# Kernel optimization log

Measured on AMD Instinct MI355X. Metric: run time of the kernel, lower is better.

The kernel has to match this reference:

```python
import jax, jax.numpy as jnp
import numpy as np

N_NODES = 262144      # 2048 graphs * 128 nodes each
NUM_GRAPHS = 2048
MAX_NODES = 128
HIDDEN = 256
OUT_CH = 12
N_EDGES = 2097152     # ~avg degree 8


def setup_inputs() -> dict:
    key = jax.random.key(0)
    k1, k2, k3, k4 = jax.random.split(key, 4)
    x = jax.random.normal(k1, (N_NODES, HIDDEN), dtype=jnp.float32)
    # xavier-ish projection weight for Linear(6*hidden -> 12)
    W = jax.random.normal(k2, (OUT_CH, 6 * HIDDEN), dtype=jnp.float32) * (1.0 / np.sqrt(6 * HIDDEN))
    b = jnp.zeros((OUT_CH,), dtype=jnp.float32)
    # uniform graphs: sorted batch ids, MAX_NODES nodes per graph
    batch = (jnp.arange(N_NODES, dtype=jnp.int32) // MAX_NODES).astype(jnp.int32)
    # edges sampled within graphs: pick graph, then two local node ids
    g = jax.random.randint(k3, (N_EDGES,), 0, NUM_GRAPHS, dtype=jnp.int32)
    loc = jax.random.randint(k4, (N_EDGES, 2), 0, MAX_NODES, dtype=jnp.int32)
    src = g * MAX_NODES + loc[:, 0]
    dst = g * MAX_NODES + loc[:, 1]
    edge_index = jnp.stack([src, dst], axis=0).astype(jnp.int32)
    return {"x": x, "W": W, "b": b, "batch": batch, "edge_index": edge_index,
            "num_graphs": NUM_GRAPHS, "max_nodes": MAX_NODES}


def reference(x, W, b, batch, edge_index, num_graphs, max_nodes):
    N, H = x.shape
    G, M = num_graphs, max_nodes
    # local index of each node within its graph (batch is sorted by graph)
    counts = jax.ops.segment_sum(jnp.ones((N,), dtype=jnp.int32), batch, num_segments=G)
    starts = jnp.cumsum(counts) - counts            # exclusive prefix sum => first node of each graph
    local = jnp.arange(N, dtype=jnp.int32) - starts[batch]
    # dense per-graph node features X [G, M, H]
    X = jnp.zeros((G, M, H), dtype=x.dtype).at[batch, local].set(x)
    # dense symmetric adjacency A [G, M, M] (assignment semantics, like the torch loop)
    gi = batch[edge_index[0]]
    li = local[edge_index[0]]
    lj = local[edge_index[1]]
    A = jnp.zeros((G, M, M), dtype=x.dtype)
    A = A.at[gi, li, lj].set(1.0)
    A = A.at[gi, lj, li].set(1.0)
    # 6-gram walk readouts
    walk = X
    vs = [walk.sum(axis=1)]                          # v1
    for _ in range(5):                               # v2..v6
        walk = jnp.einsum('gnm,gmh->gnh', A, walk) * X
        vs.append(walk.sum(axis=1))
    out = jnp.concatenate(vs, axis=-1)               # == stack(dim=1).reshape(G, 6*H)
    out = out @ W.T + b                              # n_gram_projection
    return out
```

## Files before the change

### kernel.cpp

```cpp
#include <hip/hip_runtime.h>
#include <stdint.h>

#define NGRAPH 2048
#define MNODES 128
#define HID 256
#define OUTC 12
#define NEDGE 2097152
#define NSUB 16
#define SUBCAP 160
#define CURPAD 16

typedef __attribute__((ext_vector_type(8))) short short8;
typedef __attribute__((ext_vector_type(4))) float v4f;

#define SLICE 64
#define SWT_STRIDE 136

__device__ __forceinline__ unsigned int cvtpk_bf16(float lo, float hi) {
    unsigned int r;
    asm("v_cvt_pk_bf16_f32 %0, %1, %2" : "=v"(r) : "v"(lo), "v"(hi));
    return r;
}

__global__ void scatter_edges(const int* __restrict__ ei,
                              unsigned int* __restrict__ buckets,
                              unsigned int* __restrict__ cursors) {
    int e = blockIdx.x * blockDim.x + threadIdx.x;
    if (e >= NEDGE) return;
    int sub = blockIdx.x & (NSUB - 1);
    int sN = ei[e];
    int dN = ei[NEDGE + e];
    int g = sN >> 7;
    unsigned int slot = atomicAdd(&cursors[(g * NSUB + sub) * CURPAD], 1u);
    if (slot < SUBCAP)
        buckets[((size_t)g * NSUB + sub) * SUBCAP + slot] =
            (unsigned)(sN & 127) | ((unsigned)(dN & 127) << 8);
}

__global__ void build_from_buckets(const unsigned int* __restrict__ buckets,
                                   const unsigned int* __restrict__ cursors,
                                   unsigned int* __restrict__ bits) {
    __shared__ unsigned int sb[MNODES * 4];
    int g = blockIdx.x;
    int t = threadIdx.x;
    for (int i = t; i < MNODES * 4; i += 256) sb[i] = 0;
    __syncthreads();
    int sub = t >> 4;
    int i0 = t & 15;
    unsigned int n = cursors[(g * NSUB + sub) * CURPAD];
    if (n > SUBCAP) n = SUBCAP;
    const unsigned int* bk = buckets + ((size_t)g * NSUB + sub) * SUBCAP;
    for (unsigned int i = i0; i < n; i += 16) {
        unsigned int p = bk[i];
        int li = p & 127;
        int lj = (p >> 8) & 127;
        atomicOr(&sb[li * 4 + (lj >> 5)], 1u << (lj & 31));
        atomicOr(&sb[lj * 4 + (li >> 5)], 1u << (li & 31));
    }
    __syncthreads();
    unsigned int* dst = bits + (size_t)g * (MNODES * 4);
    for (int i = t; i < MNODES * 4; i += 256) dst[i] = sb[i];
}

__global__ void build_bits(const int* __restrict__ ei, unsigned int* __restrict__ bits) {
    int e = blockIdx.x * blockDim.x + threadIdx.x;
    if (e >= NEDGE) return;
    int sN = ei[e];
    int dN = ei[NEDGE + e];
    int g = sN >> 7;
    int li = sN & 127;
    int lj = dN & 127;
    unsigned int* base = bits + (size_t)g * (MNODES * 4);
    atomicOr(&base[li * 4 + (lj >> 5)], 1u << (lj & 31));
    atomicOr(&base[lj * 4 + (li >> 5)], 1u << (li & 31));
}

__launch_bounds__(256, 3)
__global__ void walk2(const float* __restrict__ x,
                      const float* __restrict__ W,
                      const unsigned int* __restrict__ Abits,
                      float* __restrict__ partial) {
    __shared__ unsigned short sWT[2][SLICE][SWT_STRIDE];
    __shared__ float sVs2[2][6][SLICE];

    const int bx = blockIdx.x;
    const int g = bx >> 2;
    const int s = bx & 3;
    const int tid = threadIdx.x;
    const int wave = tid >> 6;
    const int lane = tid & 63;
    const int lrow = lane & 15;
    const int quad = lane >> 4;
    const int rhalf = wave >> 1;
    const int r0 = rhalf * 64;
    const int c0 = (wave & 1) * 32;
    const int cg0 = s * SLICE + c0;

    short8 areg[4][4];
    {
        const uint4* Bg = (const uint4*)(Abits + (size_t)g * (MNODES * 4));
#pragma unroll
        for (int rt = 0; rt < 4; rt++) {
            uint4 w4 = Bg[r0 + rt * 16 + lrow];
#pragma unroll
            for (int ks = 0; ks < 4; ks++) {
                unsigned int w = (ks == 0 ? w4.x : ks == 1 ? w4.y : ks == 2 ? w4.z : w4.w) >> (quad * 8);
                short8 a;
#pragma unroll
                for (int j = 0; j < 8; j++)
                    a[j] = (short)(((w >> j) & 1u) ? 0x3F80 : 0);
                areg[rt][ks] = a;
            }
        }
    }

    float xf[4][2][4];
    const float* xg = x + (size_t)g * (MNODES * HID);
#pragma unroll
    for (int rt = 0; rt < 4; rt++)
#pragma unroll
        for (int ct = 0; ct < 2; ct++) {
            int col = cg0 + ct * 16 + lrow;
#pragma unroll
            for (int reg = 0; reg < 4; reg++) {
                int row = r0 + rt * 16 + quad * 4 + reg;
                xf[rt][ct][reg] = xg[row * HID + col];
            }
        }
#pragma unroll
    for (int ct = 0; ct < 2; ct++) {
        int lcol = c0 + ct * 16 + lrow;
        float cs = 0.0f;
#pragma unroll
        for (int rt = 0; rt < 4; rt++) {
            int nbase = r0 + rt * 16 + quad * 4;
            uint2 u;
            u.x = cvtpk_bf16(xf[rt][ct][0], xf[rt][ct][1]);
            u.y = cvtpk_bf16(xf[rt][ct][2], xf[rt][ct][3]);
            *(uint2*)&sWT[0][lcol][nbase] = u;
            cs += xf[rt][ct][0] + xf[rt][ct][1] + xf[rt][ct][2] + xf[rt][ct][3];
        }
        cs += __shfl_xor(cs, 16);
        cs += __shfl_xor(cs, 32);
        if (quad == 0) sVs2[rhalf][0][lcol] = cs;
    }
    __syncthreads();

    for (int it = 1; it <= 5; it++) {
        const int cur = (it - 1) & 1;
        const int nxt = it & 1;
        v4f acc[4][2];
#pragma unroll
        for (int rt = 0; rt < 4; rt++)
#pragma unroll
            for (int ct = 0; ct < 2; ct++) acc[rt][ct] = (v4f)(0.0f);
#pragma unroll
        for (int ks = 0; ks < 4; ks++) {
            int k0 = ks * 32 + quad * 8;
#pragma unroll
            for (int ct = 0; ct < 2; ct++) {
                short8 bf = *(const short8*)&sWT[cur][c0 + ct * 16 + lrow][k0];
#pragma unroll
                for (int rt = 0; rt < 4; rt++)
                    acc[rt][ct] = __builtin_amdgcn_mfma_f32_16x16x32_bf16(areg[rt][ks], bf, acc[rt][ct], 0, 0, 0);
            }
        }
#pragma unroll
        for (int ct = 0; ct < 2; ct++) {
            int lcol = c0 + ct * 16 + lrow;
            float cs = 0.0f;
#pragma unroll
            for (int rt = 0; rt < 4; rt++) {
                float nw0 = acc[rt][ct][0] * xf[rt][ct][0];
                float nw1 = acc[rt][ct][1] * xf[rt][ct][1];
                float nw2 = acc[rt][ct][2] * xf[rt][ct][2];
                float nw3 = acc[rt][ct][3] * xf[rt][ct][3];
                int nbase = r0 + rt * 16 + quad * 4;
                uint2 u;
                u.x = cvtpk_bf16(nw0, nw1);
                u.y = cvtpk_bf16(nw2, nw3);
                *(uint2*)&sWT[nxt][lcol][nbase] = u;
                cs += nw0 + nw1 + nw2 + nw3;
            }
            cs += __shfl_xor(cs, 16);
            cs += __shfl_xor(cs, 32);
            if (quad == 0) sVs2[rhalf][it][lcol] = cs;
        }
        __syncthreads();
    }

    {
        int cbase = wave * 3;
#pragma unroll
        for (int cc = 0; cc < 3; cc++) {
            int c = cbase + cc;
            const float* wr = W + c * (6 * HID) + s * SLICE;
            float p = 0.0f;
#pragma unroll
            for (int k = 0; k < 6; k++) {
                float v = sVs2[0][k][lane] + sVs2[1][k][lane];
                p += v * wr[k * HID + lane];
            }
#pragma unroll
            for (int off = 32; off >= 1; off >>= 1) p += __shfl_down(p, off);
            if (lane == 0) partial[bx * OUTC + c] = p;
        }
    }
}

__global__ void combine(const float* __restrict__ partial, const float* __restrict__ bvec,
                        float* __restrict__ out) {
    int i = blockIdx.x * blockDim.x + threadIdx.x;
    if (i >= NGRAPH * OUTC) return;
    int c = i % OUTC;
    int g = i / OUTC;
    float p = bvec[c];
#pragma unroll
    for (int s = 0; s < 4; s++) p += partial[(g * 4 + s) * OUTC + c];
    out[i] = p;
}

extern "C" void kernel_launch(void* const* d_in, const int* in_sizes, int n_in,
                              void* d_out, int out_size, void* d_ws, size_t ws_size,
                              hipStream_t stream) {
    const float* x = (const float*)d_in[0];
    const float* W = (const float*)d_in[1];
    const float* b = (const float*)d_in[2];
    const int* ei = (const int*)d_in[4];
    float* out = (float*)d_out;

    const size_t BUCKETS = (size_t)NGRAPH * NSUB * SUBCAP * sizeof(unsigned int);
    const size_t BITS    = (size_t)NGRAPH * MNODES * 4 * sizeof(unsigned int);
    const size_t CURS    = (size_t)NGRAPH * NSUB * CURPAD * sizeof(unsigned int);
    const size_t PARTIAL = (size_t)NGRAPH * 4 * OUTC * sizeof(float);

    if (ws_size >= BUCKETS + BITS + CURS + PARTIAL) {
        unsigned int* buckets = (unsigned int*)d_ws;
        unsigned int* bits    = (unsigned int*)((char*)d_ws + BUCKETS);
        unsigned int* cursors = (unsigned int*)((char*)d_ws + BUCKETS + BITS);
        float* partial        = (float*)((char*)d_ws + BUCKETS + BITS + CURS);
        hipMemsetAsync(cursors, 0, CURS, stream);
        scatter_edges<<<NEDGE / 256, 256, 0, stream>>>(ei, buckets, cursors);
        build_from_buckets<<<NGRAPH, 256, 0, stream>>>(buckets, cursors, bits);
        walk2<<<NGRAPH * 4, 256, 0, stream>>>(x, W, bits, partial);
        combine<<<(NGRAPH * OUTC + 255) / 256, 256, 0, stream>>>(partial, b, out);
    } else {
        unsigned int* bits = (unsigned int*)d_ws;
        float* partial = (float*)((char*)d_ws + BITS);
        hipMemsetAsync(bits, 0, BITS, stream);
        build_bits<<<NEDGE / 512, 512, 0, stream>>>(ei, bits);
        walk2<<<NGRAPH * 4, 256, 0, stream>>>(x, W, bits, partial);
        combine<<<(NGRAPH * OUTC + 255) / 256, 256, 0, stream>>>(partial, b, out);
    }
}
```

Measured before the change: 490.3 us.

## Fuse adjacency bitmap build into walk kernel and use packed f32 math

Removes the separate build_from_buckets kernel. Each walk2 block now builds its graph's adjacency bitmap in shared memory from the edge buckets, reusing one sWT buffer. This drops one launch and the global bits round-trip, at the cost of each graph's buckets being read and OR-ed four times, once per column-slice block. It also switches the elementwise multiply and column sums to v_pk_mul/v_pk_add_f32 and raises wave priority around the MFMA loop with s_setprio.

```diff
diff --git a/kernel.cpp b/kernel.cpp
--- a/kernel.cpp
+++ b/kernel.cpp
@@ -12,6 +12,7 @@
 
 typedef __attribute__((ext_vector_type(8))) short short8;
 typedef __attribute__((ext_vector_type(4))) float v4f;
+typedef __attribute__((ext_vector_type(2))) float v2f;
 
 #define SLICE 64
 #define SWT_STRIDE 136
@@ -20,6 +21,12 @@
     unsigned int r;
     asm("v_cvt_pk_bf16_f32 %0, %1, %2" : "=v"(r) : "v"(lo), "v"(hi));
     return r;
+}
+__device__ __forceinline__ v2f pk_mul(v2f a, v2f b) {
+    v2f r; asm("v_pk_mul_f32 %0, %1, %2" : "=v"(r) : "v"(a), "v"(b)); return r;
+}
+__device__ __forceinline__ v2f pk_add(v2f a, v2f b) {
+    v2f r; asm("v_pk_add_f32 %0, %1, %2" : "=v"(r) : "v"(a), "v"(b)); return r;
 }
 
 __global__ void scatter_edges(const int* __restrict__ ei,
@@ -37,31 +44,6 @@
             (unsigned)(sN & 127) | ((unsigned)(dN & 127) << 8);
 }
 
-__global__ void build_from_buckets(const unsigned int* __restrict__ buckets,
-                                   const unsigned int* __restrict__ cursors,
-                                   unsigned int* __restrict__ bits) {
-    __shared__ unsigned int sb[MNODES * 4];
-    int g = blockIdx.x;
-    int t = threadIdx.x;
-    for (int i = t; i < MNODES * 4; i += 256) sb[i] = 0;
-    __syncthreads();
-    int sub = t >> 4;
-    int i0 = t & 15;
-    unsigned int n = cursors[(g * NSUB + sub) * CURPAD];
-    if (n > SUBCAP) n = SUBCAP;
-    const unsigned int* bk = buckets + ((size_t)g * NSUB + sub) * SUBCAP;
-    for (unsigned int i = i0; i < n; i += 16) {
-        unsigned int p = bk[i];
-        int li = p & 127;
-        int lj = (p >> 8) & 127;
-        atomicOr(&sb[li * 4 + (lj >> 5)], 1u << (lj & 31));
-        atomicOr(&sb[lj * 4 + (li >> 5)], 1u << (li & 31));
-    }
-    __syncthreads();
-    unsigned int* dst = bits + (size_t)g * (MNODES * 4);
-    for (int i = t; i < MNODES * 4; i += 256) dst[i] = sb[i];
-}
-
 __global__ void build_bits(const int* __restrict__ ei, unsigned int* __restrict__ bits) {
     int e = blockIdx.x * blockDim.x + threadIdx.x;
     if (e >= NEDGE) return;
@@ -78,9 +60,12 @@
 __launch_bounds__(256, 3)
 __global__ void walk2(const float* __restrict__ x,
                       const float* __restrict__ W,
+                      const unsigned int* __restrict__ buckets,
+                      const unsigned int* __restrict__ cursors,
                       const unsigned int* __restrict__ Abits,
+                      int use_bucket,
                       float* __restrict__ partial) {
-    __shared__ unsigned short sWT[2][SLICE][SWT_STRIDE];
+    __shared__ __align__(16) unsigned short sWT[2][SLICE][SWT_STRIDE];
     __shared__ float sVs2[2][6][SLICE];
 
     const int bx = blockIdx.x;
@@ -97,11 +82,29 @@
     const int cg0 = s * SLICE + c0;
 
     short8 areg[4][4];
-    {
-        const uint4* Bg = (const uint4*)(Abits + (size_t)g * (MNODES * 4));
+    if (use_bucket) {
+        unsigned int* sb = (unsigned int*)&sWT[1][0][0];
+        for (int i = tid; i < MNODES * 4; i += 256) sb[i] = 0;
+        __syncthreads();
+        {
+            int sub = tid >> 4;
+            int i0 = tid & 15;
+            unsigned int n = cursors[(g * NSUB + sub) * CURPAD];
+            if (n > SUBCAP) n = SUBCAP;
+            const unsigned int* bk = buckets + ((size_t)g * NSUB + sub) * SUBCAP;
+            for (unsigned int i = i0; i < n; i += 16) {
+                unsigned int p = bk[i];
+                int li = p & 127;
+                int lj = (p >> 8) & 127;
+                atomicOr(&sb[li * 4 + (lj >> 5)], 1u << (lj & 31));
+                atomicOr(&sb[lj * 4 + (li >> 5)], 1u << (li & 31));
+            }
+        }
+        __syncthreads();
 #pragma unroll
         for (int rt = 0; rt < 4; rt++) {
-            uint4 w4 = Bg[r0 + rt * 16 + lrow];
+            int row = r0 + rt * 16 + lrow;
+            uint4 w4 = *(const uint4*)&sb[row * 4];
 #pragma unroll
             for (int ks = 0; ks < 4; ks++) {
                 unsigned int w = (ks == 0 ? w4.x : ks == 1 ? w4.y : ks == 2 ? w4.z : w4.w) >> (quad * 8);
@@ -112,34 +115,52 @@
                 areg[rt][ks] = a;
             }
         }
-    }
-
-    float xf[4][2][4];
+    } else {
+        const uint4* Bg = (const uint4*)(Abits + (size_t)g * (MNODES * 4));
+#pragma unroll
+        for (int rt = 0; rt < 4; rt++) {
+            uint4 w4 = Bg[r0 + rt * 16 + lrow];
+#pragma unroll
+            for (int ks = 0; ks < 4; ks++) {
+                unsigned int w = (ks == 0 ? w4.x : ks == 1 ? w4.y : ks == 2 ? w4.z : w4.w) >> (quad * 8);
+                short8 a;
+#pragma unroll
+                for (int j = 0; j < 8; j++)
+                    a[j] = (short)(((w >> j) & 1u) ? 0x3F80 : 0);
+                areg[rt][ks] = a;
+            }
+        }
+    }
+
+    v2f xf2[4][2][2];
     const float* xg = x + (size_t)g * (MNODES * HID);
 #pragma unroll
     for (int rt = 0; rt < 4; rt++)
 #pragma unroll
         for (int ct = 0; ct < 2; ct++) {
             int col = cg0 + ct * 16 + lrow;
-#pragma unroll
-            for (int reg = 0; reg < 4; reg++) {
-                int row = r0 + rt * 16 + quad * 4 + reg;
-                xf[rt][ct][reg] = xg[row * HID + col];
-            }
+            int row = r0 + rt * 16 + quad * 4;
+            float l0 = xg[(row + 0) * HID + col];
+            float l1 = xg[(row + 1) * HID + col];
+            float l2 = xg[(row + 2) * HID + col];
+            float l3 = xg[(row + 3) * HID + col];
+            xf2[rt][ct][0] = (v2f){l0, l1};
+            xf2[rt][ct][1] = (v2f){l2, l3};
         }
 #pragma unroll
     for (int ct = 0; ct < 2; ct++) {
         int lcol = c0 + ct * 16 + lrow;
-        float cs = 0.0f;
+        v2f csp = (v2f)(0.0f);
 #pragma unroll
         for (int rt = 0; rt < 4; rt++) {
             int nbase = r0 + rt * 16 + quad * 4;
             uint2 u;
-            u.x = cvtpk_bf16(xf[rt][ct][0], xf[rt][ct][1]);
-            u.y = cvtpk_bf16(xf[rt][ct][2], xf[rt][ct][3]);
+            u.x = cvtpk_bf16(xf2[rt][ct][0][0], xf2[rt][ct][0][1]);
+            u.y = cvtpk_bf16(xf2[rt][ct][1][0], xf2[rt][ct][1][1]);
             *(uint2*)&sWT[0][lcol][nbase] = u;
-            cs += xf[rt][ct][0] + xf[rt][ct][1] + xf[rt][ct][2] + xf[rt][ct][3];
-        }
+            csp = pk_add(csp, pk_add(xf2[rt][ct][0], xf2[rt][ct][1]));
+        }
+        float cs = csp[0] + csp[1];
         cs += __shfl_xor(cs, 16);
         cs += __shfl_xor(cs, 32);
         if (quad == 0) sVs2[rhalf][0][lcol] = cs;
@@ -154,6 +175,7 @@
         for (int rt = 0; rt < 4; rt++)
 #pragma unroll
             for (int ct = 0; ct < 2; ct++) acc[rt][ct] = (v4f)(0.0f);
+        __builtin_amdgcn_s_setprio(1);
 #pragma unroll
         for (int ks = 0; ks < 4; ks++) {
             int k0 = ks * 32 + quad * 8;
@@ -165,23 +187,23 @@
                     acc[rt][ct] = __builtin_amdgcn_mfma_f32_16x16x32_bf16(areg[rt][ks], bf, acc[rt][ct], 0, 0, 0);
             }
         }
+        __builtin_amdgcn_s_setprio(0);
 #pragma unroll
         for (int ct = 0; ct < 2; ct++) {
             int lcol = c0 + ct * 16 + lrow;
-            float cs = 0.0f;
+            v2f csp = (v2f)(0.0f);
 #pragma unroll
             for (int rt = 0; rt < 4; rt++) {
-                float nw0 = acc[rt][ct][0] * xf[rt][ct][0];
-                float nw1 = acc[rt][ct][1] * xf[rt][ct][1];
-                float nw2 = acc[rt][ct][2] * xf[rt][ct][2];
-                float nw3 = acc[rt][ct][3] * xf[rt][ct][3];
+                v2f nw01 = pk_mul(__builtin_shufflevector(acc[rt][ct], acc[rt][ct], 0, 1), xf2[rt][ct][0]);
+                v2f nw23 = pk_mul(__builtin_shufflevector(acc[rt][ct], acc[rt][ct], 2, 3), xf2[rt][ct][1]);
                 int nbase = r0 + rt * 16 + quad * 4;
                 uint2 u;
-                u.x = cvtpk_bf16(nw0, nw1);
-                u.y = cvtpk_bf16(nw2, nw3);
+                u.x = cvtpk_bf16(nw01[0], nw01[1]);
+                u.y = cvtpk_bf16(nw23[0], nw23[1]);
                 *(uint2*)&sWT[nxt][lcol][nbase] = u;
-                cs += nw0 + nw1 + nw2 + nw3;
-            }
+                csp = pk_add(csp, pk_add(nw01, nw23));
+            }
+            float cs = csp[0] + csp[1];
             cs += __shfl_xor(cs, 16);
             cs += __shfl_xor(cs, 32);
             if (quad == 0) sVs2[rhalf][it][lcol] = cs;
@@ -230,26 +252,24 @@
     float* out = (float*)d_out;
 
     const size_t BUCKETS = (size_t)NGRAPH * NSUB * SUBCAP * sizeof(unsigned int);
+    const size_t CURS    = (size_t)NGRAPH * NSUB * CURPAD * sizeof(unsigned int);
     const size_t BITS    = (size_t)NGRAPH * MNODES * 4 * sizeof(unsigned int);
-    const size_t CURS    = (size_t)NGRAPH * NSUB * CURPAD * sizeof(unsigned int);
     const size_t PARTIAL = (size_t)NGRAPH * 4 * OUTC * sizeof(float);
 
-    if (ws_size >= BUCKETS + BITS + CURS + PARTIAL) {
+    if (ws_size >= BUCKETS + CURS + PARTIAL) {
         unsigned int* buckets = (unsigned int*)d_ws;
-        unsigned int* bits    = (unsigned int*)((char*)d_ws + BUCKETS);
-        unsigned int* cursors = (unsigned int*)((char*)d_ws + BUCKETS + BITS);
-        float* partial        = (float*)((char*)d_ws + BUCKETS + BITS + CURS);
+        unsigned int* cursors = (unsigned int*)((char*)d_ws + BUCKETS);
+        float* partial        = (float*)((char*)d_ws + BUCKETS + CURS);
         hipMemsetAsync(cursors, 0, CURS, stream);
         scatter_edges<<<NEDGE / 256, 256, 0, stream>>>(ei, buckets, cursors);
-        build_from_buckets<<<NGRAPH, 256, 0, stream>>>(buckets, cursors, bits);
-        walk2<<<NGRAPH * 4, 256, 0, stream>>>(x, W, bits, partial);
+        walk2<<<NGRAPH * 4, 256, 0, stream>>>(x, W, buckets, cursors, nullptr, 1, partial);
         combine<<<(NGRAPH * OUTC + 255) / 256, 256, 0, stream>>>(partial, b, out);
     } else {
         unsigned int* bits = (unsigned int*)d_ws;
         float* partial = (float*)((char*)d_ws + BITS);
         hipMemsetAsync(bits, 0, BITS, stream);
         build_bits<<<NEDGE / 512, 512, 0, stream>>>(ei, bits);
-        walk2<<<NGRAPH * 4, 256, 0, stream>>>(x, W, bits, partial);
+        walk2<<<NGRAPH * 4, 256, 0, stream>>>(x, W, nullptr, nullptr, bits, 0, partial);
         combine<<<(NGRAPH * OUTC + 255) / 256, 256, 0, stream>>>(partial, b, out);
     }
 }
```

Result: slower. 518.7 us (+5.8%).
